# Performance work log

Measured on AMD Instinct MI355X. Metric: run time of the kernel, lower is better.

The kernel has to match this reference:

```python
import jax, jax.numpy as jnp
import numpy as np

HEADS = 4
DIM_HEAD = 32
DIM = 128
EPS = 1e-5


def layer_norm(x, g, b):
    m = jnp.mean(x, axis=-1, keepdims=True)
    v = jnp.var(x, axis=-1, keepdims=True)
    return (x - m) * jax.lax.rsqrt(v + EPS) * g + b


def setup_inputs() -> dict:
    key = jax.random.key(0)
    ks = jax.random.split(key, 24)
    B, D, Hb, Wb = 1, DIM, 50, 50
    N, h, w = 6, 24, 44
    Q = Hb * Wb
    NK = N * h * w
    inner = HEADS * DIM_HEAD
    s = 0.02
    inp = {
        'q': jax.random.normal(ks[0], (B, D, Hb, Wb), jnp.float32),
        'k': jax.random.normal(ks[1], (B, N, D, h, w), jnp.float32),
        'v': jax.random.normal(ks[2], (B, N, D, h, w), jnp.float32),
        'W_logits': jax.random.uniform(ks[3], (B, Q, NK), jnp.float32),
        'vis': jax.random.randint(ks[4], (B, Q, NK), 0, 2, jnp.int32),
        'skip': jax.random.normal(ks[5], (B, D, Hb, Wb), jnp.float32),
        'qn_g': jnp.ones((D,)), 'qn_b': jnp.zeros((D,)),
        'kn_g': jnp.ones((D,)), 'kn_b': jnp.zeros((D,)),
        'vn_g': jnp.ones((D,)), 'vn_b': jnp.zeros((D,)),
        'wq': s * jax.random.normal(ks[6], (inner, D)), 'bq': jnp.zeros((inner,)),
        'wk': s * jax.random.normal(ks[7], (inner, D)), 'bk': jnp.zeros((inner,)),
        'wv': s * jax.random.normal(ks[8], (inner, D)), 'bv': jnp.zeros((inner,)),
        'wproj': s * jax.random.normal(ks[9], (D, inner)), 'bproj': jnp.zeros((D,)),
        'pre_g': jnp.ones((D,)), 'pre_b': jnp.zeros((D,)),
        'w1': s * jax.random.normal(ks[10], (2 * D, D)), 'b1': jnp.zeros((2 * D,)),
        'w2': s * jax.random.normal(ks[11], (D, 2 * D)), 'b2': jnp.zeros((D,)),
        'post_g': jnp.ones((D,)), 'post_b': jnp.zeros((D,)),
    }
    return inp


def reference(q, k, v, W_logits, vis, skip,
              qn_g, qn_b, kn_g, kn_b, vn_g, vn_b,
              wq, bq, wk, bk, wv, bv, wproj, bproj,
              pre_g, pre_b, w1, b1, w2, b2, post_g, post_b):
    B, D, Hb, Wb = q.shape
    Q = Hb * Wb
    scale = DIM_HEAD ** (-0.5)
    # flatten: q -> [B, Q, D]; k,v [B,N,D,h,w] -> [B, NK, D]
    qf = q.reshape(B, D, Q).transpose(0, 2, 1)
    kf = jnp.transpose(k, (0, 1, 3, 4, 2)).reshape(B, -1, D)
    vf = jnp.transpose(v, (0, 1, 3, 4, 2)).reshape(B, -1, D)
    qf = layer_norm(qf, qn_g, qn_b) @ wq.T + bq
    kf = layer_norm(kf, kn_g, kn_b) @ wk.T + bk
    vf = layer_norm(vf, vn_g, vn_b) @ wv.T + bv
    # split heads -> [B, H, Q/K, dh]
    qh = qf.reshape(B, Q, HEADS, DIM_HEAD).transpose(0, 2, 1, 3)
    kh = kf.reshape(B, -1, HEADS, DIM_HEAD).transpose(0, 2, 1, 3)
    vh = vf.reshape(B, -1, HEADS, DIM_HEAD).transpose(0, 2, 1, 3)
    logits = jnp.einsum('bhqd,bhkd->bhqk', qh, kh) * scale
    neg_inf = jnp.finfo(logits.dtype).min
    logits = jnp.where(vis[:, None] == 0, neg_inf, logits)
    logits = logits * W_logits[:, None]
    attn = jax.nn.softmax(logits, axis=-1)
    out = jnp.einsum('bhqk,bhkd->bhqd', attn, vh)
    out = out.transpose(0, 2, 1, 3).reshape(B, Q, HEADS * DIM_HEAD)
    out = out @ wproj.T + bproj
    z = out.transpose(0, 2, 1).reshape(B, D, Hb, Wb) + skip
    zf = z.reshape(B, D, Q).transpose(0, 2, 1)
    zf = layer_norm(zf, pre_g, pre_b)
    hmid = jax.nn.gelu(zf @ w1.T + b1, approximate=False)
    zf = zf + (hmid @ w2.T + b2)
    zf = layer_norm(zf, post_g, post_b)
    return zf.transpose(0, 2, 1).reshape(B, D, Hb, Wb)
```

## Files before the change

### kernel.cpp

```cpp
#include <hip/hip_runtime.h>
#include <hip/hip_bf16.h>

typedef __attribute__((ext_vector_type(8))) short bf16x8;
typedef __attribute__((ext_vector_type(4))) float f32x4;

#define NQ 2500
#define NKK 6336
#define NHEADS 4
#define DHEAD 32
#define CSC 0.25503482f
#define BIGNEG (-1.0e30f)

#define WS_QP 0
#define WS_KP 640000
#define WS_VT 2262016
#define WS_WB 3884032
#define WS_OP 4146176
#define OSPLIT_F 340000
#define OROW_F 136
#define WS_REQ3 8226176ULL
#define WS_REQ4 9586176ULL
#define WS_REQ6 12306176ULL

#define WQB 0
#define WKB 16384
#define WVB 32768
#define WPROJB 49152
#define W1B 65536
#define W2B 98304

#define NTILES_TOTAL 99
#define TQ 16
#define ATQ 32
#define TK 64
#define QBLOCKS 157
#define AQBLOCKS 79

#define KSTR 136
#define VSTR 72
#define PSTR 72
#define ABSTR 68

__device__ __forceinline__ unsigned short bf16bits(float x) {
  union { __hip_bfloat16 h; unsigned short s; } cv;
  cv.h = __float2bfloat16(x);
  return cv.s;
}

__global__ __launch_bounds__(256) void wconv_kernel(
    const float* __restrict__ wq, const float* __restrict__ wk,
    const float* __restrict__ wv, const float* __restrict__ wproj,
    const float* __restrict__ w1, const float* __restrict__ w2,
    __hip_bfloat16* __restrict__ wb)
{
  int e = (blockIdx.x * 256 + threadIdx.x) * 4;
  const float* src; int off;
  if (e < 16384)      { src = wq;    off = e; }
  else if (e < 32768) { src = wk;    off = e - 16384; }
  else if (e < 49152) { src = wv;    off = e - 32768; }
  else if (e < 65536) { src = wproj; off = e - 49152; }
  else if (e < 98304) { src = w1;    off = e - 65536; }
  else                { src = w2;    off = e - 98304; }
  float4 v = *(const float4*)(src + off);
  ushort4 o4;
  o4.x = bf16bits(v.x); o4.y = bf16bits(v.y); o4.z = bf16bits(v.z); o4.w = bf16bits(v.w);
  *(ushort4*)((unsigned short*)wb + e) = o4;
}

__global__ __launch_bounds__(256) void lnproj_kernel(
    const float* __restrict__ qin, const float* __restrict__ kin, const float* __restrict__ vin,
    const float* __restrict__ qn_g, const float* __restrict__ qn_b,
    const float* __restrict__ kn_g, const float* __restrict__ kn_b,
    const float* __restrict__ vn_g, const float* __restrict__ vn_b,
    const __hip_bfloat16* __restrict__ wball,
    const float* __restrict__ bq, const float* __restrict__ bk, const float* __restrict__ bv,
    __hip_bfloat16* __restrict__ Qp, __hip_bfloat16* __restrict__ Kp,
    __hip_bfloat16* __restrict__ Vt)
{
  __shared__ __hip_bfloat16 lxb[32][136];
  __shared__ float lpart[32][8][2];
  __shared__ float lmr[32][2];
  __shared__ float lgb[128], lbeb[128];

  const int t = threadIdx.x;
  const int bb = blockIdx.x;
  int mode, row0;
  const float *in, *g, *be, *bo;
  const __hip_bfloat16* wb;
  if (bb < 79)       { mode = 0; row0 = bb * 32;         in = qin; g = qn_g; be = qn_b; wb = wball + WQB; bo = bq; }
  else if (bb < 277) { mode = 1; row0 = (bb - 79) * 32;  in = kin; g = kn_g; be = kn_b; wb = wball + WKB; bo = bk; }
  else               { mode = 2; row0 = (bb - 277) * 32; in = vin; g = vn_g; be = vn_b; wb = wball + WVB; bo = bv; }

  if (t < 128) { lgb[t] = g[t]; lbeb[t] = be[t]; }

  const int row = t & 31, seg = t >> 5;
  int grow = row0 + row;
  size_t base, dstr;
  bool rvalid = true;
  if (mode == 0) { rvalid = (grow < NQ); base = (size_t)(rvalid ? grow : NQ - 1); dstr = NQ; }
  else { int n = grow / 1056, rr = grow - n * 1056; base = (size_t)n * 135168 + rr; dstr = 1056; }

  float xr[16];
  float s = 0.f, ss = 0.f;
  #pragma unroll
  for (int i = 0; i < 16; ++i) {
    float x = in[base + (size_t)(seg * 16 + i) * dstr];
    xr[i] = x; s += x; ss += x * x;
  }
  lpart[row][seg][0] = s; lpart[row][seg][1] = ss;
  __syncthreads();
  if (t < 32) {
    float S = 0.f, SS = 0.f;
    #pragma unroll
    for (int j = 0; j < 8; ++j) { S += lpart[t][j][0]; SS += lpart[t][j][1]; }
    float mean = S * (1.f / 128.f);
    float var  = SS * (1.f / 128.f) - mean * mean;
    lmr[t][0] = mean;
    lmr[t][1] = rsqrtf(fmaxf(var, 0.f) + 1e-5f);
  }
  __syncthreads();
  {
    float mean = lmr[row][0], rstd = lmr[row][1];
    #pragma unroll
    for (int i = 0; i < 16; ++i) {
      int d = seg * 16 + i;
      lxb[row][d] = __float2bfloat16((xr[i] - mean) * rstd * lgb[d] + lbeb[d]);
    }
  }
  __syncthreads();

  const int wid = t >> 6, lane = t & 63;
  const int n16 = lane & 15, quad = lane >> 4;
  const int ow = wid * 32;

  f32x4 acc[2][2] = {};
  for (int kt = 0; kt < 4; ++kt) {
    bf16x8 af[2];
    #pragma unroll
    for (int mi = 0; mi < 2; ++mi)
      af[mi] = *(const bf16x8*)&lxb[mi * 16 + n16][kt * 32 + quad * 8];
    #pragma unroll
    for (int ni = 0; ni < 2; ++ni) {
      bf16x8 bw = *(const bf16x8*)(wb + (size_t)(ow + ni * 16 + n16) * 128 + kt * 32 + quad * 8);
      #pragma unroll
      for (int mi = 0; mi < 2; ++mi)
        acc[mi][ni] = __builtin_amdgcn_mfma_f32_16x16x32_bf16(af[mi], bw, acc[mi][ni], 0, 0, 0);
    }
  }

  float bias[2];
  #pragma unroll
  for (int ni = 0; ni < 2; ++ni) bias[ni] = bo[ow + ni * 16 + n16];

  #pragma unroll
  for (int mi = 0; mi < 2; ++mi) {
    int gr0 = row0 + mi * 16 + quad * 4;
    if (mode == 2) {
      #pragma unroll
      for (int ni = 0; ni < 2; ++ni) {
        int o = ow + ni * 16 + n16;
        ushort4 v4;
        v4.x = bf16bits(acc[mi][ni][0] + bias[ni]);
        v4.y = bf16bits(acc[mi][ni][1] + bias[ni]);
        v4.z = bf16bits(acc[mi][ni][2] + bias[ni]);
        v4.w = bf16bits(acc[mi][ni][3] + bias[ni]);
        *(ushort4*)((unsigned short*)Vt + (size_t)o * NKK + gr0) = v4;
      }
    } else {
      #pragma unroll
      for (int rg = 0; rg < 4; ++rg) {
        int gr = gr0 + rg;
        if (mode != 0 || gr < NQ) {
          #pragma unroll
          for (int ni = 0; ni < 2; ++ni) {
            int o = ow + ni * 16 + n16;
            __hip_bfloat16 b16 = __float2bfloat16(acc[mi][ni][rg] + bias[ni]);
            if (mode == 0) Qp[(size_t)gr * 128 + o] = b16;
            else           Kp[(size_t)gr * 128 + o] = b16;
          }
        }
      }
    }
  }
}

__global__ __launch_bounds__(256, 2) void attn_kernel(
    const __hip_bfloat16* __restrict__ Qp,
    const __hip_bfloat16* __restrict__ Kp,
    const __hip_bfloat16* __restrict__ Vt,
    const float* __restrict__ Wl,
    const int* __restrict__ vis,
    float* __restrict__ Opart)
{
  __shared__ alignas(16) __hip_bfloat16 lk[TK * KSTR];
  __shared__ alignas(16) __hip_bfloat16 lv[128 * VSTR];
  __shared__ alignas(16) float sc[ATQ * ABSTR];
  __shared__ alignas(16) __hip_bfloat16 lp[NHEADS * ATQ * PSTR];

  const int t = threadIdx.x;
  const int lane = t & 63;
  const int h = t >> 6;
  const int n16 = lane & 15;
  const int quad = lane >> 4;
  const int q0 = blockIdx.x * ATQ;
  const int split = blockIdx.y;
  const int ksplit = gridDim.y;
  const int tstart = (NTILES_TOTAL * split) / ksplit;
  const int ntiles = (NTILES_TOTAL * (split + 1)) / ksplit - tstart;

  bf16x8 aq[2];
  #pragma unroll
  for (int m = 0; m < 2; ++m) {
    int gqa = q0 + m * 16 + n16; if (gqa >= NQ) gqa = NQ - 1;
    aq[m] = *(const bf16x8*)(Qp + (size_t)gqa * 128 + h * DHEAD + quad * 8);
  }

  const int kr = t >> 2, kc = (t & 3) * 32;
  const int vr = t >> 1, vc = (t & 1) * 32;
  const int qq = t >> 3, kkc = (t & 7) * 8;
  int gqe = q0 + qq; if (gqe >= NQ) gqe = NQ - 1;
  const size_t wbase = (size_t)gqe * NKK + kkc;

  bf16x8 bones;
  {
    short one = (short)0x3F80;
    short val = (n16 == 0) ? one : (short)0;
    #pragma unroll
    for (int j = 0; j < 8; ++j) bones[j] = val;
  }

  uint4 pk0, pk1, pk2, pk3, pv0, pv1, pv2, pv3;
  float4 pw0, pw1; int4 pvs0, pvs1;

  auto issue = [&](int tile) {
    int k0 = (tstart + tile) * TK;
    const uint4* ksrc = (const uint4*)(Kp + (size_t)(k0 + kr) * 128 + kc);
    pk0 = ksrc[0]; pk1 = ksrc[1]; pk2 = ksrc[2]; pk3 = ksrc[3];
    const uint4* vsrc = (const uint4*)(Vt + (size_t)vr * NKK + k0 + vc);
    pv0 = vsrc[0]; pv1 = vsrc[1]; pv2 = vsrc[2]; pv3 = vsrc[3];
    pw0  = *(const float4*)(Wl + wbase + k0);
    pw1  = *(const float4*)(Wl + wbase + k0 + 4);
    pvs0 = *(const int4*)(vis + wbase + k0);
    pvs1 = *(const int4*)(vis + wbase + k0 + 4);
  };
  auto commit = [&]() {
    uint4* kd = (uint4*)&lk[kr * KSTR + kc];
    kd[0] = pk0; kd[1] = pk1; kd[2] = pk2; kd[3] = pk3;
    uint4* vd = (uint4*)&lv[vr * VSTR + vc];
    vd[0] = pv0; vd[1] = pv1; vd[2] = pv2; vd[3] = pv3;
    float4 c0, c1;
    c0.x = pvs0.x ? pw0.x * CSC : BIGNEG * pw0.x;
    c0.y = pvs0.y ? pw0.y * CSC : BIGNEG * pw0.y;
    c0.z = pvs0.z ? pw0.z * CSC : BIGNEG * pw0.z;
    c0.w = pvs0.w ? pw0.w * CSC : BIGNEG * pw0.w;
    c1.x = pvs1.x ? pw1.x * CSC : BIGNEG * pw1.x;
    c1.y = pvs1.y ? pw1.y * CSC : BIGNEG * pw1.y;
    c1.z = pvs1.z ? pw1.z * CSC : BIGNEG * pw1.z;
    c1.w = pvs1.w ? pw1.w * CSC : BIGNEG * pw1.w;
    *(float4*)&sc[qq * ABSTR + kkc] = c0;
    *(float4*)&sc[qq * ABSTR + kkc + 4] = c1;
  };

  f32x4 o[2][3];
  #pragma unroll
  for (int m = 0; m < 2; ++m)
    #pragma unroll
    for (int j = 0; j < 3; ++j)
      o[m][j] = f32x4{0.f, 0.f, 0.f, 0.f};

  issue(0);
  commit();
  __syncthreads();

  for (int kt = 0; kt < ntiles; ++kt) {
    if (kt + 1 < ntiles) issue(kt + 1);

    f32x4 s[2][4];
    #pragma unroll
    for (int ks = 0; ks < 4; ++ks) {
      bf16x8 bk = *(const bf16x8*)&lk[(ks * 16 + n16) * KSTR + h * DHEAD + quad * 8];
      f32x4 z = {0.f, 0.f, 0.f, 0.f};
      s[0][ks] = __builtin_amdgcn_mfma_f32_16x16x32_bf16(aq[0], bk, z, 0, 0, 0);
      s[1][ks] = __builtin_amdgcn_mfma_f32_16x16x32_bf16(aq[1], bk, z, 0, 0, 0);
    }
    #pragma unroll
    for (int m = 0; m < 2; ++m) {
      #pragma unroll
      for (int ks = 0; ks < 4; ++ks) {
        #pragma unroll
        for (int r = 0; r < 4; ++r) {
          int row = m * 16 + quad * 4 + r;
          float c = sc[row * ABSTR + ks * 16 + n16];
          float tt = s[m][ks][r] * c;
          float arg = (c >= 0.f) ? tt : c;
          float p = exp2f(fminf(arg, 60.f));
          lp[h * (ATQ * PSTR) + row * PSTR + ks * 16 + n16] = __float2bfloat16(p);
        }
      }
    }
    #pragma unroll
    for (int kk = 0; kk < 2; ++kk) {
      bf16x8 bv0 = *(const bf16x8*)&lv[(h * DHEAD + n16) * VSTR + kk * 32 + quad * 8];
      bf16x8 bv1 = *(const bf16x8*)&lv[(h * DHEAD + 16 + n16) * VSTR + kk * 32 + quad * 8];
      #pragma unroll
      for (int m = 0; m < 2; ++m) {
        bf16x8 ap = *(const bf16x8*)&lp[h * (ATQ * PSTR) + (m * 16 + n16) * PSTR + kk * 32 + quad * 8];
        o[m][0] = __builtin_amdgcn_mfma_f32_16x16x32_bf16(ap, bv0, o[m][0], 0, 0, 0);
        o[m][1] = __builtin_amdgcn_mfma_f32_16x16x32_bf16(ap, bv1, o[m][1], 0, 0, 0);
        o[m][2] = __builtin_amdgcn_mfma_f32_16x16x32_bf16(ap, bones, o[m][2], 0, 0, 0);
      }
    }

    if (kt + 1 < ntiles) {
      __syncthreads();
      commit();
      __syncthreads();
    }
  }

  #pragma unroll
  for (int m = 0; m < 2; ++m) {
    #pragma unroll
    for (int r = 0; r < 4; ++r) {
      int gq = q0 + m * 16 + quad * 4 + r;
      if (gq < NQ) {
        float* rowp = Opart + (size_t)split * OSPLIT_F + (size_t)gq * OROW_F;
        rowp[h * DHEAD + n16] = o[m][0][r];
        rowp[h * DHEAD + 16 + n16] = o[m][1][r];
        if (n16 == 0) rowp[128 + h] = o[m][2][r];
      }
    }
  }
}

__global__ __launch_bounds__(256) void mlp_kernel(
    const float* __restrict__ Opart, int ksplit,
    const float* __restrict__ skip,
    const __hip_bfloat16* __restrict__ wball,
    const float* __restrict__ bproj,
    const float* __restrict__ pre_g, const float* __restrict__ pre_b,
    const float* __restrict__ b1, const float* __restrict__ b2,
    const float* __restrict__ post_g, const float* __restrict__ post_b,
    float* __restrict__ out)
{
  __shared__ __hip_bfloat16 sab[16][136];
  __shared__ __hip_bfloat16 znb[16][136];
  __shared__ float znf[16][132];
  __shared__ __hip_bfloat16 hb[16][264];
  __shared__ float part[16][4][2];

  const __hip_bfloat16* wprojb = wball + WPROJB;
  const __hip_bfloat16* w1b    = wball + W1B;
  const __hip_bfloat16* w2b    = wball + W2B;

  const int t = threadIdx.x;
  const int q0 = blockIdx.x * TQ;

  {
    int row = t >> 4, c0 = (t & 15) * 8;
    int gq = q0 + row; int cq = gq < NQ ? gq : NQ - 1;
    int head = c0 >> 5;
    float ll = 0.f;
    float acc8[8] = {};
    for (int s = 0; s < ksplit; ++s) {
      const float* rp = Opart + (size_t)s * OSPLIT_F + (size_t)cq * OROW_F;
      ll += rp[128 + head];
      float4 a = *(const float4*)(rp + c0);
      float4 b = *(const float4*)(rp + c0 + 4);
      acc8[0] += a.x; acc8[1] += a.y; acc8[2] += a.z; acc8[3] += a.w;
      acc8[4] += b.x; acc8[5] += b.y; acc8[6] += b.z; acc8[7] += b.w;
    }
    float rll = 1.f / fmaxf(ll, 1e-30f);
    #pragma unroll
    for (int i = 0; i < 8; ++i)
      sab[row][c0 + i] = __float2bfloat16(acc8[i] * rll);
  }
  __syncthreads();

  const int wid = t >> 6, lane = t & 63;
  const int n16 = lane & 15, quad = lane >> 4;
  const int qrow0 = q0 + quad * 4;

  f32x4 acc1[2] = {};
  for (int kt = 0; kt < 4; ++kt) {
    bf16x8 af = *(const bf16x8*)&sab[n16][kt * 32 + quad * 8];
    #pragma unroll
    for (int ni = 0; ni < 2; ++ni) {
      int o = wid * 32 + ni * 16 + n16;
      bf16x8 bw = *(const bf16x8*)(wprojb + (size_t)o * 128 + kt * 32 + quad * 8);
      acc1[ni] = __builtin_amdgcn_mfma_f32_16x16x32_bf16(af, bw, acc1[ni], 0, 0, 0);
    }
  }
  float z[2][4];
  #pragma unroll
  for (int ni = 0; ni < 2; ++ni) {
    int o = wid * 32 + ni * 16 + n16;
    float bo = bproj[o];
    if (qrow0 + 3 < NQ) {
      float4 sk = *(const float4*)(skip + (size_t)o * NQ + qrow0);
      z[ni][0] = acc1[ni][0] + bo + sk.x;
      z[ni][1] = acc1[ni][1] + bo + sk.y;
      z[ni][2] = acc1[ni][2] + bo + sk.z;
      z[ni][3] = acc1[ni][3] + bo + sk.w;
    } else {
      #pragma unroll
      for (int rg = 0; rg < 4; ++rg) {
        int cq = qrow0 + rg < NQ ? qrow0 + rg : NQ - 1;
        z[ni][rg] = acc1[ni][rg] + bo + skip[(size_t)o * NQ + cq];
      }
    }
  }
  #pragma unroll
  for (int rg = 0; rg < 4; ++rg) {
    float s = z[0][rg] + z[1][rg];
    float ss = z[0][rg] * z[0][rg] + z[1][rg] * z[1][rg];
    s += __shfl_xor(s, 1);  ss += __shfl_xor(ss, 1);
    s += __shfl_xor(s, 2);  ss += __shfl_xor(ss, 2);
    s += __shfl_xor(s, 4);  ss += __shfl_xor(ss, 4);
    s += __shfl_xor(s, 8);  ss += __shfl_xor(ss, 8);
    if (n16 == 0) { part[quad * 4 + rg][wid][0] = s; part[quad * 4 + rg][wid][1] = ss; }
  }
  __syncthreads();
  #pragma unroll
  for (int rg = 0; rg < 4; ++rg) {
    int row = quad * 4 + rg;
    float S  = part[row][0][0] + part[row][1][0] + part[row][2][0] + part[row][3][0];
    float SS = part[row][0][1] + part[row][1][1] + part[row][2][1] + part[row][3][1];
    float mean = S * (1.f / 128.f);
    float var  = SS * (1.f / 128.f) - mean * mean;
    float rstd = rsqrtf(fmaxf(var, 0.f) + 1e-5f);
    #pragma unroll
    for (int ni = 0; ni < 2; ++ni) {
      int o = wid * 32 + ni * 16 + n16;
      float zn = (z[ni][rg] - mean) * rstd * pre_g[o] + pre_b[o];
      znf[row][o] = zn;
      znb[row][o] = __float2bfloat16(zn);
    }
  }
  __syncthreads();

  f32x4 acc2[4] = {};
  for (int kt = 0; kt < 4; ++kt) {
    bf16x8 af = *(const bf16x8*)&znb[n16][kt * 32 + quad * 8];
    #pragma unroll
    for (int ni = 0; ni < 4; ++ni) {
      int j = wid * 64 + ni * 16 + n16;
      bf16x8 bw = *(const bf16x8*)(w1b + (size_t)j * 128 + kt * 32 + quad * 8);
      acc2[ni] = __builtin_amdgcn_mfma_f32_16x16x32_bf16(af, bw, acc2[ni], 0, 0, 0);
    }
  }
  #pragma unroll
  for (int ni = 0; ni < 4; ++ni) {
    int j = wid * 64 + ni * 16 + n16;
    float bj = b1[j];
    #pragma unroll
    for (int rg = 0; rg < 4; ++rg) {
      float a1 = acc2[ni][rg] + bj;
      hb[quad * 4 + rg][j] = __float2bfloat16(0.5f * a1 * (1.0f + erff(a1 * 0.70710678118654752f)));
    }
  }
  __syncthreads();

  f32x4 acc3[2] = {};
  for (int kt = 0; kt < 8; ++kt) {
    bf16x8 af = *(const bf16x8*)&hb[n16][kt * 32 + quad * 8];
    #pragma unroll
    for (int ni = 0; ni < 2; ++ni) {
      int o = wid * 32 + ni * 16 + n16;
      bf16x8 bw = *(const bf16x8*)(w2b + (size_t)o * 256 + kt * 32 + quad * 8);
      acc3[ni] = __builtin_amdgcn_mfma_f32_16x16x32_bf16(af, bw, acc3[ni], 0, 0, 0);
    }
  }
  float y[2][4];
  #pragma unroll
  for (int ni = 0; ni < 2; ++ni) {
    int o = wid * 32 + ni * 16 + n16;
    float bo = b2[o];
    #pragma unroll
    for (int rg = 0; rg < 4; ++rg)
      y[ni][rg] = znf[quad * 4 + rg][o] + acc3[ni][rg] + bo;
  }
  #pragma unroll
  for (int rg = 0; rg < 4; ++rg) {
    float s = y[0][rg] + y[1][rg];
    float ss = y[0][rg] * y[0][rg] + y[1][rg] * y[1][rg];
    s += __shfl_xor(s, 1);  ss += __shfl_xor(ss, 1);
    s += __shfl_xor(s, 2);  ss += __shfl_xor(ss, 2);
    s += __shfl_xor(s, 4);  ss += __shfl_xor(ss, 4);
    s += __shfl_xor(s, 8);  ss += __shfl_xor(ss, 8);
    if (n16 == 0) { part[quad * 4 + rg][wid][0] = s; part[quad * 4 + rg][wid][1] = ss; }
  }
  __syncthreads();
  #pragma unroll
  for (int rg = 0; rg < 4; ++rg) {
    int row = quad * 4 + rg;
    float S  = part[row][0][0] + part[row][1][0] + part[row][2][0] + part[row][3][0];
    float SS = part[row][0][1] + part[row][1][1] + part[row][2][1] + part[row][3][1];
    float mean = S * (1.f / 128.f);
    float var  = SS * (1.f / 128.f) - mean * mean;
    float rstd = rsqrtf(fmaxf(var, 0.f) + 1e-5f);
    #pragma unroll
    for (int ni = 0; ni < 2; ++ni) {
      int o = wid * 32 + ni * 16 + n16;
      y[ni][rg] = (y[ni][rg] - mean) * rstd * post_g[o] + post_b[o];
    }
  }
  #pragma unroll
  for (int ni = 0; ni < 2; ++ni) {
    int o = wid * 32 + ni * 16 + n16;
    if (qrow0 + 3 < NQ) {
      *(float4*)(out + (size_t)o * NQ + qrow0) = make_float4(y[ni][0], y[ni][1], y[ni][2], y[ni][3]);
    } else {
      #pragma unroll
      for (int rg = 0; rg < 4; ++rg)
        if (qrow0 + rg < NQ) out[(size_t)o * NQ + qrow0 + rg] = y[ni][rg];
    }
  }
}

extern "C" void kernel_launch(void* const* d_in, const int* in_sizes, int n_in,
                              void* d_out, int out_size, void* d_ws, size_t ws_size,
                              hipStream_t stream) {
  if (ws_size < WS_REQ3) return;
  const int ksplit = (ws_size >= WS_REQ6) ? 6 : (ws_size >= WS_REQ4) ? 4 : 3;

  const float* q     = (const float*)d_in[0];
  const float* k     = (const float*)d_in[1];
  const float* v     = (const float*)d_in[2];
  const float* Wl    = (const float*)d_in[3];
  const int*   vis   = (const int*)d_in[4];
  const float* skip  = (const float*)d_in[5];
  const float* qn_g  = (const float*)d_in[6];
  const float* qn_b  = (const float*)d_in[7];
  const float* kn_g  = (const float*)d_in[8];
  const float* kn_b  = (const float*)d_in[9];
  const float* vn_g  = (const float*)d_in[10];
  const float* vn_b  = (const float*)d_in[11];
  const float* wq    = (const float*)d_in[12];
  const float* bq    = (const float*)d_in[13];
  const float* wk    = (const float*)d_in[14];
  const float* bk    = (const float*)d_in[15];
  const float* wv    = (const float*)d_in[16];
  const float* bv    = (const float*)d_in[17];
  const float* wproj = (const float*)d_in[18];
  const float* bproj = (const float*)d_in[19];
  const float* pre_g = (const float*)d_in[20];
  const float* pre_b = (const float*)d_in[21];
  const float* w1    = (const float*)d_in[22];
  const float* b1    = (const float*)d_in[23];
  const float* w2    = (const float*)d_in[24];
  const float* b2    = (const float*)d_in[25];
  const float* post_g= (const float*)d_in[26];
  const float* post_b= (const float*)d_in[27];

  char* ws = (char*)d_ws;
  __hip_bfloat16* Qp = (__hip_bfloat16*)(ws + WS_QP);
  __hip_bfloat16* Kp = (__hip_bfloat16*)(ws + WS_KP);
  __hip_bfloat16* Vt = (__hip_bfloat16*)(ws + WS_VT);
  __hip_bfloat16* Wb = (__hip_bfloat16*)(ws + WS_WB);
  float* Opart = (float*)(ws + WS_OP);

  hipLaunchKernelGGL(wconv_kernel, dim3(128), dim3(256), 0, stream,
                     wq, wk, wv, wproj, w1, w2, Wb);

  hipLaunchKernelGGL(lnproj_kernel, dim3(475), dim3(256), 0, stream,
                     q, k, v, qn_g, qn_b, kn_g, kn_b, vn_g, vn_b,
                     Wb, bq, bk, bv, Qp, Kp, Vt);

  hipLaunchKernelGGL(attn_kernel, dim3(AQBLOCKS, ksplit), dim3(256), 0, stream,
                     Qp, Kp, Vt, Wl, vis, Opart);

  hipLaunchKernelGGL(mlp_kernel, dim3(QBLOCKS), dim3(256), 0, stream,
                     Opart, ksplit, skip, Wb, bproj, pre_g, pre_b,
                     b1, b2, post_g, post_b, (float*)d_out);
}
```

Baseline: 244.8 us.

## Load K/V fragments directly from global, double-buffer score scales, raise occupancy

The attention kernel stops staging K and V tiles through LDS and instead loads the MFMA B-operand fragments straight from global memory (relying on L2/L1 reuse across blocks and waves). The mask/weight scale buffer is double-buffered, which removes one barrier per tile. The smaller LDS footprint allows launch bounds of 4 blocks per SM, and the key-split count now scales with workspace size up to 12. The cost is more uncoalesced global traffic per wave and loads that sit on the critical path, since they are no longer prefetched a tile ahead.

```diff
diff --git a/kernel.cpp b/kernel.cpp
--- a/kernel.cpp
+++ b/kernel.cpp
@@ -19,8 +19,6 @@
 #define OSPLIT_F 340000
 #define OROW_F 136
 #define WS_REQ3 8226176ULL
-#define WS_REQ4 9586176ULL
-#define WS_REQ6 12306176ULL
 
 #define WQB 0
 #define WKB 16384
@@ -36,8 +34,6 @@
 #define QBLOCKS 157
 #define AQBLOCKS 79
 
-#define KSTR 136
-#define VSTR 72
 #define PSTR 72
 #define ABSTR 68
 
@@ -184,7 +180,7 @@
   }
 }
 
-__global__ __launch_bounds__(256, 2) void attn_kernel(
+__global__ __launch_bounds__(256, 4) void attn_kernel(
     const __hip_bfloat16* __restrict__ Qp,
     const __hip_bfloat16* __restrict__ Kp,
     const __hip_bfloat16* __restrict__ Vt,
@@ -192,9 +188,7 @@
     const int* __restrict__ vis,
     float* __restrict__ Opart)
 {
-  __shared__ alignas(16) __hip_bfloat16 lk[TK * KSTR];
-  __shared__ alignas(16) __hip_bfloat16 lv[128 * VSTR];
-  __shared__ alignas(16) float sc[ATQ * ABSTR];
+  __shared__ alignas(16) float sc[2][ATQ * ABSTR];
   __shared__ alignas(16) __hip_bfloat16 lp[NHEADS * ATQ * PSTR];
 
   const int t = threadIdx.x;
@@ -215,8 +209,6 @@
     aq[m] = *(const bf16x8*)(Qp + (size_t)gqa * 128 + h * DHEAD + quad * 8);
   }
 
-  const int kr = t >> 2, kc = (t & 3) * 32;
-  const int vr = t >> 1, vc = (t & 1) * 32;
   const int qq = t >> 3, kkc = (t & 7) * 8;
   int gqe = q0 + qq; if (gqe >= NQ) gqe = NQ - 1;
   const size_t wbase = (size_t)gqe * NKK + kkc;
@@ -229,25 +221,16 @@
     for (int j = 0; j < 8; ++j) bones[j] = val;
   }
 
-  uint4 pk0, pk1, pk2, pk3, pv0, pv1, pv2, pv3;
   float4 pw0, pw1; int4 pvs0, pvs1;
 
   auto issue = [&](int tile) {
     int k0 = (tstart + tile) * TK;
-    const uint4* ksrc = (const uint4*)(Kp + (size_t)(k0 + kr) * 128 + kc);
-    pk0 = ksrc[0]; pk1 = ksrc[1]; pk2 = ksrc[2]; pk3 = ksrc[3];
-    const uint4* vsrc = (const uint4*)(Vt + (size_t)vr * NKK + k0 + vc);
-    pv0 = vsrc[0]; pv1 = vsrc[1]; pv2 = vsrc[2]; pv3 = vsrc[3];
     pw0  = *(const float4*)(Wl + wbase + k0);
     pw1  = *(const float4*)(Wl + wbase + k0 + 4);
     pvs0 = *(const int4*)(vis + wbase + k0);
     pvs1 = *(const int4*)(vis + wbase + k0 + 4);
   };
-  auto commit = [&]() {
-    uint4* kd = (uint4*)&lk[kr * KSTR + kc];
-    kd[0] = pk0; kd[1] = pk1; kd[2] = pk2; kd[3] = pk3;
-    uint4* vd = (uint4*)&lv[vr * VSTR + vc];
-    vd[0] = pv0; vd[1] = pv1; vd[2] = pv2; vd[3] = pv3;
+  auto commit = [&](int buf) {
     float4 c0, c1;
     c0.x = pvs0.x ? pw0.x * CSC : BIGNEG * pw0.x;
     c0.y = pvs0.y ? pw0.y * CSC : BIGNEG * pw0.y;
@@ -257,8 +240,8 @@
     c1.y = pvs1.y ? pw1.y * CSC : BIGNEG * pw1.y;
     c1.z = pvs1.z ? pw1.z * CSC : BIGNEG * pw1.z;
     c1.w = pvs1.w ? pw1.w * CSC : BIGNEG * pw1.w;
-    *(float4*)&sc[qq * ABSTR + kkc] = c0;
-    *(float4*)&sc[qq * ABSTR + kkc + 4] = c1;
+    *(float4*)&sc[buf][qq * ABSTR + kkc] = c0;
+    *(float4*)&sc[buf][qq * ABSTR + kkc + 4] = c1;
   };
 
   f32x4 o[2][3];
@@ -269,20 +252,30 @@
       o[m][j] = f32x4{0.f, 0.f, 0.f, 0.f};
 
   issue(0);
-  commit();
+  commit(0);
   __syncthreads();
 
   for (int kt = 0; kt < ntiles; ++kt) {
+    const int k0 = (tstart + kt) * TK;
+    const int cur = kt & 1;
     if (kt + 1 < ntiles) issue(kt + 1);
 
     f32x4 s[2][4];
     #pragma unroll
     for (int ks = 0; ks < 4; ++ks) {
-      bf16x8 bk = *(const bf16x8*)&lk[(ks * 16 + n16) * KSTR + h * DHEAD + quad * 8];
+      bf16x8 bk = *(const bf16x8*)(Kp + (size_t)(k0 + ks * 16 + n16) * 128 + h * DHEAD + quad * 8);
       f32x4 z = {0.f, 0.f, 0.f, 0.f};
       s[0][ks] = __builtin_amdgcn_mfma_f32_16x16x32_bf16(aq[0], bk, z, 0, 0, 0);
       s[1][ks] = __builtin_amdgcn_mfma_f32_16x16x32_bf16(aq[1], bk, z, 0, 0, 0);
     }
+
+    bf16x8 bv[2][2];
+    #pragma unroll
+    for (int kk = 0; kk < 2; ++kk) {
+      bv[kk][0] = *(const bf16x8*)(Vt + (size_t)(h * DHEAD + n16) * NKK + k0 + kk * 32 + quad * 8);
+      bv[kk][1] = *(const bf16x8*)(Vt + (size_t)(h * DHEAD + 16 + n16) * NKK + k0 + kk * 32 + quad * 8);
+    }
+
     #pragma unroll
     for (int m = 0; m < 2; ++m) {
       #pragma unroll
@@ -290,7 +283,7 @@
         #pragma unroll
         for (int r = 0; r < 4; ++r) {
           int row = m * 16 + quad * 4 + r;
-          float c = sc[row * ABSTR + ks * 16 + n16];
+          float c = sc[cur][row * ABSTR + ks * 16 + n16];
           float tt = s[m][ks][r] * c;
           float arg = (c >= 0.f) ? tt : c;
           float p = exp2f(fminf(arg, 60.f));
@@ -298,22 +291,20 @@
         }
       }
     }
+
     #pragma unroll
     for (int kk = 0; kk < 2; ++kk) {
-      bf16x8 bv0 = *(const bf16x8*)&lv[(h * DHEAD + n16) * VSTR + kk * 32 + quad * 8];
-      bf16x8 bv1 = *(const bf16x8*)&lv[(h * DHEAD + 16 + n16) * VSTR + kk * 32 + quad * 8];
       #pragma unroll
       for (int m = 0; m < 2; ++m) {
         bf16x8 ap = *(const bf16x8*)&lp[h * (ATQ * PSTR) + (m * 16 + n16) * PSTR + kk * 32 + quad * 8];
-        o[m][0] = __builtin_amdgcn_mfma_f32_16x16x32_bf16(ap, bv0, o[m][0], 0, 0, 0);
-        o[m][1] = __builtin_amdgcn_mfma_f32_16x16x32_bf16(ap, bv1, o[m][1], 0, 0, 0);
+        o[m][0] = __builtin_amdgcn_mfma_f32_16x16x32_bf16(ap, bv[kk][0], o[m][0], 0, 0, 0);
+        o[m][1] = __builtin_amdgcn_mfma_f32_16x16x32_bf16(ap, bv[kk][1], o[m][1], 0, 0, 0);
         o[m][2] = __builtin_amdgcn_mfma_f32_16x16x32_bf16(ap, bones, o[m][2], 0, 0, 0);
       }
     }
 
     if (kt + 1 < ntiles) {
-      __syncthreads();
-      commit();
+      commit(cur ^ 1);
       __syncthreads();
     }
   }
@@ -522,7 +513,9 @@
                               void* d_out, int out_size, void* d_ws, size_t ws_size,
                               hipStream_t stream) {
   if (ws_size < WS_REQ3) return;
-  const int ksplit = (ws_size >= WS_REQ6) ? 6 : (ws_size >= WS_REQ4) ? 4 : 3;
+  int ksplit = (int)((ws_size - WS_OP) / (size_t)(OSPLIT_F * 4));
+  if (ksplit > 12) ksplit = 12;
+  if (ksplit < 3)  ksplit = 3;
 
   const float* q     = (const float*)d_in[0];
   const float* k     = (const float*)d_in[1];
```

New measurement: 248.1 us. No clear change (+1.4%).
